# Kernel tuning notes

Hardware: AMD Instinct MI355X
Metric: run time of the kernel (lower is better)

The kernel has to match this reference:

```python
import jax, jax.numpy as jnp
import numpy as np

N_NODES = 100000
N_EDGES = 1600000
DIM = 128


def setup_inputs() -> dict:
    key = jax.random.key(0)
    k1, k2, k3, k4 = jax.random.split(key, 4)
    x = jax.random.normal(k1, (N_NODES, DIM), dtype=jnp.float32)
    edge_index = jax.random.randint(k2, (2, N_EDGES), 0, N_NODES, dtype=jnp.int64)
    # PyG GCNConv params: Linear weight [out, in] (glorot) and bias [out] (zeros -> use small randn for a non-trivial grad path)
    W = jax.random.normal(k3, (DIM, DIM), dtype=jnp.float32) * (1.0 / np.sqrt(DIM))
    b = jax.random.normal(k4, (DIM,), dtype=jnp.float32) * 0.01
    return {"x": x, "edge_index": edge_index, "W": W, "b": b}


def reference(x, edge_index, W, b):
    # Faithful GCNConv: add self-loops, symmetric deg^-1/2 normalization,
    # linear transform, scatter-add aggregation, bias.
    N = x.shape[0]
    loop = jnp.arange(N, dtype=edge_index.dtype)
    src = jnp.concatenate([edge_index[0], loop])  # [E+N]
    dst = jnp.concatenate([edge_index[1], loop])  # [E+N]

    # degree (with self-loops) on destination nodes
    deg = jax.ops.segment_sum(jnp.ones_like(dst, dtype=x.dtype), dst, num_segments=N)
    dinv = jnp.where(deg > 0, jax.lax.rsqrt(deg), 0.0)
    norm = dinv[src] * dinv[dst]  # [E+N]

    x_lin = x @ W.T  # [N, dim] — PyG applies linear before propagate
    msg = x_lin[src] * norm[:, None]  # [E+N, dim] gather + scale
    out = jax.ops.segment_sum(msg, dst, num_segments=N)  # scatter-add aggregate
    return out + b
```

## Files before the change

### kernel.cpp

```cpp
#include <hip/hip_runtime.h>
#include <hip/hip_bf16.h>


#define DIM 128
#define BINSHIFT 9
#define BINSZ 512
#define MAXNB 256
#define WSTRIDE 136

typedef __attribute__((ext_vector_type(8))) short short8;
typedef __attribute__((ext_vector_type(4))) float f32x4;

__device__ inline unsigned short f2bf(float f) {
    unsigned u = __builtin_bit_cast(unsigned, f);
    return (unsigned short)((u + 0x7FFFu + ((u >> 16) & 1u)) >> 16);
}

__device__ inline float4 bf4_to_f4(uint2 u) {
    float4 r;
    r.x = __builtin_bit_cast(float, u.x << 16);
    r.y = __builtin_bit_cast(float, u.x & 0xFFFF0000u);
    r.z = __builtin_bit_cast(float, u.y << 16);
    r.w = __builtin_bit_cast(float, u.y & 0xFFFF0000u);
    return r;
}


__global__ void zero_hist(int* __restrict__ hist) {
    hist[threadIdx.x] = 0;
}

__global__ __launch_bounds__(256) void bin_hist(const int* __restrict__ dst, int E,
                                                int* __restrict__ hist, int nb) {
    __shared__ int lh[MAXNB];
    int t = threadIdx.x;
    lh[t] = 0;
    __syncthreads();
    int chunk = (E + gridDim.x - 1) / gridDim.x;
    int base = blockIdx.x * chunk, end = min(E, base + chunk);
    for (int i = base + t; i < end; i += 256)
        atomicAdd(&lh[dst[i] >> BINSHIFT], 1);
    __syncthreads();
    if (t < nb && lh[t]) atomicAdd(&hist[t], lh[t]);
}

__global__ __launch_bounds__(256) void bin_scan(const int* __restrict__ hist,
                                                int* __restrict__ binStart,
                                                int* __restrict__ binCursor,
                                                int* __restrict__ row_ptr,
                                                int nb, int N) {
    __shared__ int sa[MAXNB], sb[MAXNB];
    int t = threadIdx.x;
    sa[t] = (t < nb) ? hist[t] : 0;
    __syncthreads();
    int* src = sa; int* dstp = sb;
    for (int step = 1; step < MAXNB; step <<= 1) {
        int v = src[t];
        if (t >= step) v += src[t - step];
        dstp[t] = v;
        __syncthreads();
        int* tmp = src; src = dstp; dstp = tmp;
    }
    if (t < nb) {
        int excl = src[t] - hist[t];
        binStart[t] = excl;
        binCursor[t] = excl;
    }
    if (t == nb - 1) binStart[nb] = src[t];
    if (t == 0) row_ptr[N] = src[nb - 1];
}

__global__ __launch_bounds__(256) void bin_scatter(const int* __restrict__ ei, int E,
                                                   int* __restrict__ binCursor,
                                                   int2* __restrict__ binned, int nb) {
    __shared__ int lh[MAXNB];
    __shared__ int lbase[MAXNB];
    int t = threadIdx.x;
    lh[t] = 0;
    __syncthreads();
    int chunk = (E + gridDim.x - 1) / gridDim.x;
    int base = blockIdx.x * chunk, end = min(E, base + chunk);
    for (int i = base + t; i < end; i += 256)
        atomicAdd(&lh[ei[E + i] >> BINSHIFT], 1);
    __syncthreads();
    if (t < nb) {
        int c = lh[t];
        lbase[t] = c ? atomicAdd(&binCursor[t], c) : 0;
        lh[t] = 0;
    }
    __syncthreads();
    for (int i = base + t; i < end; i += 256) {
        int s = ei[i], d = ei[E + i];
        int b = d >> BINSHIFT;
        int pos = lbase[b] + atomicAdd(&lh[b], 1);
        binned[pos] = make_int2(s, d);
    }
}

__global__ __launch_bounds__(256) void csr_build(const int2* __restrict__ binned,
                                                 const int* __restrict__ binStart,
                                                 int* __restrict__ col,
                                                 int* __restrict__ row_ptr,
                                                 float* __restrict__ dinv, int N) {
    __shared__ int ldeg[BINSZ];
    __shared__ int sa[BINSZ], sb[BINSZ];
    __shared__ int lcur[BINSZ];
    int t = threadIdx.x, b = blockIdx.x;
    int s0 = binStart[b], s1 = binStart[b + 1];
    for (int i = t; i < BINSZ; i += 256) { ldeg[i] = 0; lcur[i] = 0; }
    __syncthreads();
    for (int i = s0 + t; i < s1; i += 256)
        atomicAdd(&ldeg[binned[i].y & (BINSZ - 1)], 1);
    __syncthreads();
    for (int i = t; i < BINSZ; i += 256) sa[i] = ldeg[i];
    __syncthreads();
    int* src = sa; int* dstp = sb;
    for (int step = 1; step < BINSZ; step <<= 1) {
        for (int i = t; i < BINSZ; i += 256) {
            int v = src[i];
            if (i >= step) v += src[i - step];
            dstp[i] = v;
        }
        __syncthreads();
        int* tmp = src; src = dstp; dstp = tmp;
    }
    for (int i = t; i < BINSZ; i += 256) dstp[i] = src[i] - ldeg[i];
    __syncthreads();
    for (int i = t; i < BINSZ; i += 256) {
        int n = (b << BINSHIFT) + i;
        if (n < N) {
            row_ptr[n] = s0 + dstp[i];
            dinv[n] = rsqrtf((float)(ldeg[i] + 1));
        }
    }
    for (int i = s0 + t; i < s1; i += 256) {
        int2 e = binned[i];
        int li = e.y & (BINSZ - 1);
        col[s0 + dstp[li] + atomicAdd(&lcur[li], 1)] = e.x;
    }
}


__global__ __launch_bounds__(256) void gemm_mfma(const float* __restrict__ x,
                                                 const float* __restrict__ W,
                                                 unsigned short* __restrict__ xlin, int N) {
    __shared__ unsigned short wbf[DIM * WSTRIDE];
    __shared__ unsigned short obuf[4 * 16 * WSTRIDE];
    int t = threadIdx.x;

    for (int it = 0; it < 16; ++it) {
        int f = it * 256 + t;
        int j = f >> 5;
        int kq = f & 31;
        float4 w4 = ((const float4*)W)[f];
        unsigned short* p = &wbf[j * WSTRIDE + kq * 4];
        p[0] = f2bf(w4.x); p[1] = f2bf(w4.y); p[2] = f2bf(w4.z); p[3] = f2bf(w4.w);
    }
    __syncthreads();

    int wid = t >> 6, lane = t & 63;
    int m = lane & 15, quad = lane >> 4;
    int row_base = blockIdx.x * 64 + wid * 16;

    f32x4 acc[8];
#pragma unroll
    for (int j = 0; j < 8; ++j) acc[j] = (f32x4){0.f, 0.f, 0.f, 0.f};

    int arow = row_base + m;
    if (arow >= N) arow = N - 1;
    const float* xr = x + (size_t)arow * DIM + quad * 8;

#pragma unroll
    for (int kc = 0; kc < 4; ++kc) {
        float4 a0 = *(const float4*)(xr + kc * 32);
        float4 a1 = *(const float4*)(xr + kc * 32 + 4);
        short8 af;
        af[0] = (short)f2bf(a0.x); af[1] = (short)f2bf(a0.y);
        af[2] = (short)f2bf(a0.z); af[3] = (short)f2bf(a0.w);
        af[4] = (short)f2bf(a1.x); af[5] = (short)f2bf(a1.y);
        af[6] = (short)f2bf(a1.z); af[7] = (short)f2bf(a1.w);
#pragma unroll
        for (int jt = 0; jt < 8; ++jt) {
            short8 bf = *(const short8*)&wbf[(jt * 16 + m) * WSTRIDE + kc * 32 + quad * 8];
            acc[jt] = __builtin_amdgcn_mfma_f32_16x16x32_bf16(af, bf, acc[jt], 0, 0, 0);
        }
    }

    unsigned short* ob = &obuf[wid * 16 * WSTRIDE];
#pragma unroll
    for (int jt = 0; jt < 8; ++jt)
#pragma unroll
        for (int r = 0; r < 4; ++r)
            ob[(quad * 4 + r) * WSTRIDE + jt * 16 + m] = f2bf(acc[jt][r]);
#pragma unroll
    for (int it = 0; it < 4; ++it) {
        int idx = it * 64 + lane;
        int r = idx >> 4;
        int cb = idx & 15;
        int grow = row_base + r;
        if (grow < N) {
            short8 v = *(const short8*)&ob[r * WSTRIDE + cb * 8];
            *(short8*)(xlin + (size_t)grow * DIM + cb * 8) = v;
        }
    }
}


__global__ __launch_bounds__(256) void aggregate(const unsigned short* __restrict__ xlin,
                                                 const int* __restrict__ col,
                                                 const int* __restrict__ row_ptr,
                                                 const float* __restrict__ dinv,
                                                 const float* __restrict__ bias,
                                                 float* __restrict__ out, int N) {
    int node = blockIdx.x * 8 + (threadIdx.x >> 5);
    int lane = threadIdx.x & 31;
    if (node >= N) return;

    float di = dinv[node];
    int r0 = row_ptr[node], r1 = row_ptr[node + 1];

    const uint2* xl = (const uint2*)xlin;
    float4 a = bf4_to_f4(xl[(size_t)node * 32 + lane]);
    float4 acc = make_float4(di * a.x, di * a.y, di * a.z, di * a.w);

    for (int i = r0; i < r1; ++i) {
        int s = col[i];
        float ds = dinv[s];
        float4 v = bf4_to_f4(xl[(size_t)s * 32 + lane]);
        acc.x = fmaf(ds, v.x, acc.x);
        acc.y = fmaf(ds, v.y, acc.y);
        acc.z = fmaf(ds, v.z, acc.z);
        acc.w = fmaf(ds, v.w, acc.w);
    }

    float4 bb = ((const float4*)bias)[lane];
    float4 o = make_float4(di * acc.x + bb.x, di * acc.y + bb.y,
                           di * acc.z + bb.z, di * acc.w + bb.w);
    ((float4*)out)[(size_t)node * 32 + lane] = o;
}


extern "C" void kernel_launch(void* const* d_in, const int* in_sizes, int n_in,
                              void* d_out, int out_size, void* d_ws, size_t ws_size,
                              hipStream_t stream) {
    const float* x    = (const float*)d_in[0];
    const int*   ei   = (const int*)d_in[1];
    const float* W    = (const float*)d_in[2];
    const float* bias = (const float*)d_in[3];
    float* out = (float*)d_out;

    const int N = in_sizes[0] / DIM;
    const int E = in_sizes[1] / 2;
    const int nb = (N + BINSZ - 1) >> BINSHIFT;

    char* ws = (char*)d_ws;
    size_t off = 0;
    auto alloc = [&](size_t bytes) { size_t o = off; off = (off + bytes + 255) & ~(size_t)255; return o; };
    unsigned short* xlin = (unsigned short*)(ws + alloc((size_t)N * DIM * 2));
    int2* binned   = (int2*) (ws + alloc((size_t)E * 8));
    int*  col      = (int*)  (ws + alloc((size_t)E * 4));
    int*  row_ptr  = (int*)  (ws + alloc((size_t)(N + 1) * 4));
    float* dinv    = (float*)(ws + alloc((size_t)N * 4));
    int*  hist     = (int*)  (ws + alloc(MAXNB * 4));
    int*  binStart = (int*)  (ws + alloc((MAXNB + 1) * 4));
    int*  binCursor= (int*)  (ws + alloc(MAXNB * 4));

    zero_hist<<<1, MAXNB, 0, stream>>>(hist);
    bin_hist<<<256, 256, 0, stream>>>(ei + E, E, hist, nb);
    bin_scan<<<1, MAXNB, 0, stream>>>(hist, binStart, binCursor, row_ptr, nb, N);
    bin_scatter<<<256, 256, 0, stream>>>(ei, E, binCursor, binned, nb);
    csr_build<<<nb, 256, 0, stream>>>(binned, binStart, col, row_ptr, dinv, N);
    gemm_mfma<<<(N + 63) / 64, 256, 0, stream>>>(x, W, xlin, N);
    aggregate<<<(N + 7) / 8, 256, 0, stream>>>(xlin, col, row_ptr, dinv, bias, out, N);
}
```

Baseline: 270.9 us.

## Fuse edge binning scatter into GEMM launch and widen aggregate gathers

Merges the bin_scatter pass into the GEMM kernel as extra leading blocks, so edge binning and the dense transform run concurrently in one launch and one launch is dropped. The aggregate kernel now uses 16 lanes per node, each loading 16-byte bf16 vectors, and unrolls the neighbour loop by four to keep more gathers in flight. The zero kernel is replaced by hipMemsetAsync. Risks are load imbalance between the two block types in the fused launch and higher register use per thread in aggregate.

```diff
diff --git a/kernel.cpp b/kernel.cpp
--- a/kernel.cpp
+++ b/kernel.cpp
@@ -7,6 +7,7 @@
 #define BINSZ 512
 #define MAXNB 256
 #define WSTRIDE 136
+#define SCAT_BLOCKS 256
 
 typedef __attribute__((ext_vector_type(8))) short short8;
 typedef __attribute__((ext_vector_type(4))) float f32x4;
@@ -16,19 +17,17 @@
     return (unsigned short)((u + 0x7FFFu + ((u >> 16) & 1u)) >> 16);
 }
 
-__device__ inline float4 bf4_to_f4(uint2 u) {
-    float4 r;
-    r.x = __builtin_bit_cast(float, u.x << 16);
-    r.y = __builtin_bit_cast(float, u.x & 0xFFFF0000u);
-    r.z = __builtin_bit_cast(float, u.y << 16);
-    r.w = __builtin_bit_cast(float, u.y & 0xFFFF0000u);
-    return r;
-}
-
-
-__global__ void zero_hist(int* __restrict__ hist) {
-    hist[threadIdx.x] = 0;
-}
+__device__ inline void bf8_axpy(uint4 v, float s, float* acc) {
+    acc[0] = fmaf(s, __builtin_bit_cast(float, v.x << 16), acc[0]);
+    acc[1] = fmaf(s, __builtin_bit_cast(float, v.x & 0xFFFF0000u), acc[1]);
+    acc[2] = fmaf(s, __builtin_bit_cast(float, v.y << 16), acc[2]);
+    acc[3] = fmaf(s, __builtin_bit_cast(float, v.y & 0xFFFF0000u), acc[3]);
+    acc[4] = fmaf(s, __builtin_bit_cast(float, v.z << 16), acc[4]);
+    acc[5] = fmaf(s, __builtin_bit_cast(float, v.z & 0xFFFF0000u), acc[5]);
+    acc[6] = fmaf(s, __builtin_bit_cast(float, v.w << 16), acc[6]);
+    acc[7] = fmaf(s, __builtin_bit_cast(float, v.w & 0xFFFF0000u), acc[7]);
+}
+
 
 __global__ __launch_bounds__(256) void bin_hist(const int* __restrict__ dst, int E,
                                                 int* __restrict__ hist, int nb) {
@@ -68,33 +67,6 @@
     }
     if (t == nb - 1) binStart[nb] = src[t];
     if (t == 0) row_ptr[N] = src[nb - 1];
-}
-
-__global__ __launch_bounds__(256) void bin_scatter(const int* __restrict__ ei, int E,
-                                                   int* __restrict__ binCursor,
-                                                   int2* __restrict__ binned, int nb) {
-    __shared__ int lh[MAXNB];
-    __shared__ int lbase[MAXNB];
-    int t = threadIdx.x;
-    lh[t] = 0;
-    __syncthreads();
-    int chunk = (E + gridDim.x - 1) / gridDim.x;
-    int base = blockIdx.x * chunk, end = min(E, base + chunk);
-    for (int i = base + t; i < end; i += 256)
-        atomicAdd(&lh[ei[E + i] >> BINSHIFT], 1);
-    __syncthreads();
-    if (t < nb) {
-        int c = lh[t];
-        lbase[t] = c ? atomicAdd(&binCursor[t], c) : 0;
-        lh[t] = 0;
-    }
-    __syncthreads();
-    for (int i = base + t; i < end; i += 256) {
-        int s = ei[i], d = ei[E + i];
-        int b = d >> BINSHIFT;
-        int pos = lbase[b] + atomicAdd(&lh[b], 1);
-        binned[pos] = make_int2(s, d);
-    }
 }
 
 __global__ __launch_bounds__(256) void csr_build(const int2* __restrict__ binned,
@@ -141,12 +113,40 @@
 }
 
 
-__global__ __launch_bounds__(256) void gemm_mfma(const float* __restrict__ x,
-                                                 const float* __restrict__ W,
-                                                 unsigned short* __restrict__ xlin, int N) {
+__global__ __launch_bounds__(256) void gemm_scatter(const float* __restrict__ x,
+                                                    const float* __restrict__ W,
+                                                    unsigned short* __restrict__ xlin, int N,
+                                                    const int* __restrict__ ei, int E,
+                                                    int* __restrict__ binCursor,
+                                                    int2* __restrict__ binned, int nb) {
     __shared__ unsigned short wbf[DIM * WSTRIDE];
     __shared__ unsigned short obuf[4 * 16 * WSTRIDE];
     int t = threadIdx.x;
+
+    if (blockIdx.x < SCAT_BLOCKS) {
+        int* lh = (int*)wbf;
+        int* lbase = lh + MAXNB;
+        lh[t] = 0;
+        __syncthreads();
+        int chunk = (E + SCAT_BLOCKS - 1) / SCAT_BLOCKS;
+        int base = blockIdx.x * chunk, end = min(E, base + chunk);
+        for (int i = base + t; i < end; i += 256)
+            atomicAdd(&lh[ei[E + i] >> BINSHIFT], 1);
+        __syncthreads();
+        if (t < nb) {
+            int c = lh[t];
+            lbase[t] = c ? atomicAdd(&binCursor[t], c) : 0;
+            lh[t] = 0;
+        }
+        __syncthreads();
+        for (int i = base + t; i < end; i += 256) {
+            int s = ei[i], d = ei[E + i];
+            int b = d >> BINSHIFT;
+            int pos = lbase[b] + atomicAdd(&lh[b], 1);
+            binned[pos] = make_int2(s, d);
+        }
+        return;
+    }
 
     for (int it = 0; it < 16; ++it) {
         int f = it * 256 + t;
@@ -160,7 +160,7 @@
 
     int wid = t >> 6, lane = t & 63;
     int m = lane & 15, quad = lane >> 4;
-    int row_base = blockIdx.x * 64 + wid * 16;
+    int row_base = (blockIdx.x - SCAT_BLOCKS) * 64 + wid * 16;
 
     f32x4 acc[8];
 #pragma unroll
@@ -212,31 +212,44 @@
                                                  const float* __restrict__ dinv,
                                                  const float* __restrict__ bias,
                                                  float* __restrict__ out, int N) {
-    int node = blockIdx.x * 8 + (threadIdx.x >> 5);
-    int lane = threadIdx.x & 31;
+    int node = blockIdx.x * 16 + (threadIdx.x >> 4);
+    int lane = threadIdx.x & 15;
     if (node >= N) return;
 
     float di = dinv[node];
     int r0 = row_ptr[node], r1 = row_ptr[node + 1];
 
-    const uint2* xl = (const uint2*)xlin;
-    float4 a = bf4_to_f4(xl[(size_t)node * 32 + lane]);
-    float4 acc = make_float4(di * a.x, di * a.y, di * a.z, di * a.w);
-
-    for (int i = r0; i < r1; ++i) {
+    const uint4* xl = (const uint4*)xlin;
+    float acc[8] = {};
+    bf8_axpy(xl[(size_t)node * 16 + lane], di, acc);
+
+    int i = r0;
+    for (; i + 4 <= r1; i += 4) {
+        int s0 = col[i], s1 = col[i + 1], s2 = col[i + 2], s3 = col[i + 3];
+        float d0 = dinv[s0], d1 = dinv[s1], d2 = dinv[s2], d3 = dinv[s3];
+        uint4 v0 = xl[(size_t)s0 * 16 + lane];
+        uint4 v1 = xl[(size_t)s1 * 16 + lane];
+        uint4 v2 = xl[(size_t)s2 * 16 + lane];
+        uint4 v3 = xl[(size_t)s3 * 16 + lane];
+        bf8_axpy(v0, d0, acc);
+        bf8_axpy(v1, d1, acc);
+        bf8_axpy(v2, d2, acc);
+        bf8_axpy(v3, d3, acc);
+    }
+    for (; i < r1; ++i) {
         int s = col[i];
-        float ds = dinv[s];
-        float4 v = bf4_to_f4(xl[(size_t)s * 32 + lane]);
-        acc.x = fmaf(ds, v.x, acc.x);
-        acc.y = fmaf(ds, v.y, acc.y);
-        acc.z = fmaf(ds, v.z, acc.z);
-        acc.w = fmaf(ds, v.w, acc.w);
-    }
-
-    float4 bb = ((const float4*)bias)[lane];
-    float4 o = make_float4(di * acc.x + bb.x, di * acc.y + bb.y,
-                           di * acc.z + bb.z, di * acc.w + bb.w);
-    ((float4*)out)[(size_t)node * 32 + lane] = o;
+        bf8_axpy(xl[(size_t)s * 16 + lane], dinv[s], acc);
+    }
+
+    const float4* b4 = (const float4*)(bias + lane * 8);
+    float4 bl = b4[0], bh = b4[1];
+    float4 olo = make_float4(di * acc[0] + bl.x, di * acc[1] + bl.y,
+                             di * acc[2] + bl.z, di * acc[3] + bl.w);
+    float4 ohi = make_float4(di * acc[4] + bh.x, di * acc[5] + bh.y,
+                             di * acc[6] + bh.z, di * acc[7] + bh.w);
+    float4* op = (float4*)(out + (size_t)node * DIM + lane * 8);
+    op[0] = olo;
+    op[1] = ohi;
 }
 
 
@@ -265,11 +278,11 @@
     int*  binStart = (int*)  (ws + alloc((MAXNB + 1) * 4));
     int*  binCursor= (int*)  (ws + alloc(MAXNB * 4));
 
-    zero_hist<<<1, MAXNB, 0, stream>>>(hist);
+    hipMemsetAsync(hist, 0, MAXNB * 4, stream);
     bin_hist<<<256, 256, 0, stream>>>(ei + E, E, hist, nb);
     bin_scan<<<1, MAXNB, 0, stream>>>(hist, binStart, binCursor, row_ptr, nb, N);
-    bin_scatter<<<256, 256, 0, stream>>>(ei, E, binCursor, binned, nb);
+    gemm_scatter<<<SCAT_BLOCKS + (N + 63) / 64, 256, 0, stream>>>(
+        x, W, xlin, N, ei, E, binCursor, binned, nb);
     csr_build<<<nb, 256, 0, stream>>>(binned, binStart, col, row_ptr, dinv, N);
-    gemm_mfma<<<(N + 63) / 64, 256, 0, stream>>>(x, W, xlin, N);
-    aggregate<<<(N + 7) / 8, 256, 0, stream>>>(xlin, col, row_ptr, dinv, bias, out, N);
-}
+    aggregate<<<(N + 15) / 16, 256, 0, stream>>>(xlin, col, row_ptr, dinv, bias, out, N);
+}
```

Result: faster. 232.5 us (-14.2%).
